# Optimization experiments

Hardware: AMD Instinct MI355X
Metric: run time of the kernel (lower is better)

## Reference

```python
import jax, jax.numpy as jnp
import numpy as np

V, E, H, B, T = 32000, 256, 512, 64, 24

def setup_inputs() -> dict:
    key = jax.random.key(0)
    ks = jax.random.split(key, 24)
    def n(k, shape, s=0.02):
        return jax.random.normal(k, shape, dtype=jnp.float32) * s
    inp = {
        "question_feat": n(ks[0], (B, H), 1.0),
        "image_feat": n(ks[1], (B, H), 1.0),
        "answer_seq": jax.random.randint(ks[2], (B, T), 0, V),
        "embedding": n(ks[3], (V, E)),
        "attn_W": n(ks[4], (H, 3 * H)),
        "attn_b": jnp.zeros((H,), jnp.float32),
        "v_W": n(ks[5], (1, H)),
        "fc_W": n(ks[6], (V, H)),
        "fc_b": jnp.zeros((V,), jnp.float32),
    }
    in_sizes = [E + 2 * H, H, H]  # layer0 sees cat(embed, context)=1280
    for l in range(3):
        inp[f"W_ih{l}"] = n(ks[7 + 4 * l], (4 * H, in_sizes[l]))
        inp[f"W_hh{l}"] = n(ks[8 + 4 * l], (4 * H, H))
        inp[f"b_ih{l}"] = jnp.zeros((4 * H,), jnp.float32)
        inp[f"b_hh{l}"] = jnp.zeros((4 * H,), jnp.float32)
    return inp

def _lstm_cell(x, h, c, W_ih, W_hh, b_ih, b_hh):
    # torch gate order: i, f, g, o
    g = x @ W_ih.T + b_ih + h @ W_hh.T + b_hh
    i, f, gg, o = jnp.split(g, 4, axis=-1)
    c_new = jax.nn.sigmoid(f) * c + jax.nn.sigmoid(i) * jnp.tanh(gg)
    h_new = jax.nn.sigmoid(o) * jnp.tanh(c_new)
    return h_new, c_new

def reference(question_feat, image_feat, answer_seq, embedding, attn_W, attn_b, v_W,
              fc_W, fc_b,
              W_ih0, W_hh0, b_ih0, b_hh0,
              W_ih1, W_hh1, b_ih1, b_hh1,
              W_ih2, W_hh2, b_ih2, b_hh2):
    combined = jnp.concatenate([question_feat, image_feat], axis=1)  # [B, 2H]
    x = embedding[answer_seq]            # [B, T, E]
    xs = jnp.swapaxes(x, 0, 1)           # [T, B, E]
    Ws = ((W_ih0, W_hh0, b_ih0, b_hh0),
          (W_ih1, W_hh1, b_ih1, b_hh1),
          (W_ih2, W_hh2, b_ih2, b_hh2))

    def step(carry, x_t):
        h, c, prev_attn = carry          # h, c: [3, B, H]; prev_attn: [B, H]
        energy = jnp.tanh(jnp.concatenate([prev_attn, combined], axis=1) @ attn_W.T + attn_b)
        aw = jax.nn.softmax(energy @ v_W.T, axis=1)  # [B, 1] (softmax over singleton, faithful to source)
        ctx = aw * combined                          # [B, 2H]
        cur = jnp.concatenate([x_t, ctx], axis=1)    # [B, E+2H]
        hs, cs = [], []
        for l in range(3):
            nh, nc = _lstm_cell(cur, h[l], c[l], *Ws[l])
            hs.append(nh); cs.append(nc); cur = nh
        logits = cur @ fc_W.T + fc_b                 # [B, V]
        return (jnp.stack(hs), jnp.stack(cs), cur), logits

    hdim = question_feat.shape[1]
    bsz = question_feat.shape[0]
    h0 = jnp.zeros((3, bsz, hdim), question_feat.dtype)
    c0 = jnp.zeros((3, bsz, hdim), question_feat.dtype)
    _, outs = jax.lax.scan(step, (h0, c0, question_feat), xs)
    return jnp.swapaxes(outs, 0, 1)  # [B, T, V]
```

## Files before the change

### kernel.cpp

```cpp
#include <hip/hip_runtime.h>
#include <hip/hip_bf16.h>
#include <stdint.h>


typedef short bf16x8 __attribute__((ext_vector_type(8)));
typedef float f32x4 __attribute__((ext_vector_type(4)));

#define NLSTM 96
#define NTILE_N 250
#define HSLOT 32768

__device__ __forceinline__ unsigned short f2b(float f) {
    uint32_t u = __builtin_bit_cast(uint32_t, f);
    uint32_t r = u + 0x7FFFu + ((u >> 16) & 1u);
    return (unsigned short)(r >> 16);
}
__device__ __forceinline__ float fsig(float x) {
    float e = __expf(-x);
    return __builtin_amdgcn_rcpf(1.0f + e);
}
__device__ __forceinline__ float ftanh(float x) {
    float e = __expf(-2.0f * x);
    return (1.0f - e) * __builtin_amdgcn_rcpf(1.0f + e);
}

__global__ __launch_bounds__(256) void prep(
    const float* __restrict__ Whh0,
    const float* __restrict__ Wih1, const float* __restrict__ Whh1,
    const float* __restrict__ Wih2, const float* __restrict__ Whh2,
    unsigned short* __restrict__ Wpk,
    const float* __restrict__ qf,
    const float* __restrict__ imf,
    const int* __restrict__ seq,
    const float* __restrict__ emb,
    unsigned short* __restrict__ X,
    unsigned int* __restrict__ flags,
    unsigned short* __restrict__ hst)
{
    int gid = blockIdx.x;
    int tid = threadIdx.x;
    if (gid < 6144) {
        int layer = gid / (32 * 64);
        int rem = gid % (32 * 64);
        int lbid = rem >> 6, r = rem & 63;
        int q = r >> 4, jj = r & 15;
        int grow = q * 512 + lbid * 16 + jj;
        int K = (layer == 0) ? 512 : 1024;
        size_t wbase = (layer == 0) ? 0
                     : (layer == 1) ? (size_t)32 * 64 * 512
                                    : (size_t)32 * 64 * 512 + (size_t)32 * 64 * 1024;
        unsigned short* dst = Wpk + wbase + ((size_t)lbid * 64 + r) * K;
        const float *s0, *s1 = nullptr;
        if (layer == 0)      { s0 = Whh0 + (size_t)grow * 512; }
        else if (layer == 1) { s0 = Wih1 + (size_t)grow * 512; s1 = Whh1 + (size_t)grow * 512; }
        else                 { s0 = Wih2 + (size_t)grow * 512; s1 = Whh2 + (size_t)grow * 512; }
        int half = tid >> 7, k4 = tid & 127;
        const float* src = (half == 0) ? s0 : s1;
        if (src) {
            f32x4 v = *(const f32x4*)&src[k4 * 4];
            unsigned short o[4];
            #pragma unroll
            for (int j = 0; j < 4; ++j) o[j] = f2b(v[j]);
            *(uint64_t*)&dst[half * 512 + k4 * 4] = *(uint64_t*)o;
        }
    } else if (gid < 7680) {
        int r = gid - 6144;
        int t = r >> 6, b = r & 63;
        int tok = seq[b * 24 + t];
        for (int e = tid; e < 1280; e += 256) {
            float v;
            if (e < 256)      v = emb[(size_t)tok * 256 + e];
            else if (e < 768) v = qf[b * 512 + (e - 256)];
            else              v = imf[b * 512 + (e - 768)];
            X[(size_t)r * 1280 + e] = f2b(v);
        }
    } else {
        int z = (gid - 7680) * 256 + tid;
        for (int i = z; i < 2304; i += 2048) flags[i] = 0u;
        unsigned int* h32 = (unsigned int*)hst;
        for (int l = 0; l < 3; ++l) {
            unsigned int* base = h32 + (size_t)l * 25 * (HSLOT / 2);
            for (int i = z; i < HSLOT / 2; i += 2048) base[i] = 0u;
        }
    }
}

__global__ __launch_bounds__(256) void gemm128(
    const unsigned short* __restrict__ A, int lda,
    const float* __restrict__ Wf, int ldb,
    int K,
    const float* __restrict__ bias0,
    const float* __restrict__ bias1,
    float* __restrict__ outf, int ldo, int mblocks, int xcdq)
{
    __shared__ unsigned short lA[128 * 72];
    __shared__ unsigned short lB[128 * 72];
    int lin = blockIdx.x;
    int wg = (lin & 7) * xcdq + (lin >> 3);
    const int m0 = (wg % mblocks) * 128, n0 = (wg / mblocks) * 128;
    const int tid = threadIdx.x;
    const int lane = tid & 63, wid = tid >> 6;
    const int wm = wid >> 1, wn = wid & 1;

    f32x4 acc[4][4] = {};

    for (int kt = 0; kt < K; kt += 64) {
        #pragma unroll
        for (int c = 0; c < 4; ++c) {
            int chunk = tid + c * 256;
            int row = chunk >> 3, kc = (chunk & 7) * 8;
            *(bf16x8*)&lA[row * 72 + kc] =
                *(const bf16x8*)&A[(size_t)(m0 + row) * lda + kt + kc];
            const float* bp = &Wf[(size_t)(n0 + row) * ldb + kt + kc];
            f32x4 v0 = *(const f32x4*)bp;
            f32x4 v1 = *(const f32x4*)(bp + 4);
            unsigned short o[8];
            #pragma unroll
            for (int x = 0; x < 4; ++x) { o[x] = f2b(v0[x]); o[4 + x] = f2b(v1[x]); }
            *(bf16x8*)&lB[row * 72 + kc] = *(bf16x8*)o;
        }
        __syncthreads();
        #pragma unroll
        for (int ks = 0; ks < 64; ks += 32) {
            int kl = ks + ((lane >> 4) << 3);
            bf16x8 af[4], bfr[4];
            #pragma unroll
            for (int i = 0; i < 4; ++i)
                af[i] = *(const bf16x8*)&lA[(wm * 64 + i * 16 + (lane & 15)) * 72 + kl];
            #pragma unroll
            for (int j = 0; j < 4; ++j)
                bfr[j] = *(const bf16x8*)&lB[(wn * 64 + j * 16 + (lane & 15)) * 72 + kl];
            #pragma unroll
            for (int i = 0; i < 4; ++i)
                #pragma unroll
                for (int j = 0; j < 4; ++j)
                    acc[i][j] = __builtin_amdgcn_mfma_f32_16x16x32_bf16(
                        af[i], bfr[j], acc[i][j], 0, 0, 0);
        }
        __syncthreads();
    }

    #pragma unroll
    for (int i = 0; i < 4; ++i) {
        #pragma unroll
        for (int j = 0; j < 4; ++j) {
            int n = n0 + wn * 64 + j * 16 + (lane & 15);
            float bias = bias0[n] + bias1[n];
            #pragma unroll
            for (int r = 0; r < 4; ++r) {
                int m = m0 + wm * 64 + i * 16 + ((lane >> 4) << 2) + r;
                outf[(size_t)m * ldo + n] = acc[i][j][r] + bias;
            }
        }
    }
}

#define ISSUE_CHUNK(buf, kb0)                                                 \
    {                                                                         \
        _Pragma("unroll")                                                     \
        for (int u_ = 0; u_ < 8; ++u_) {                                      \
            int kg_ = (kb0) + u_ * 32 + lk;                                   \
            const unsigned short* hb_ = (kg_ < 512) ? A0 : A1;                \
            int kk_ = kg_ & 511;                                              \
            const unsigned short* ap_ =                                       \
                hb_ + ((kk_ >> 4) << 10) + brow16 + (kk_ & 15);               \
            asm volatile("global_load_dwordx4 %0, %1, off"                    \
                         : "=v"(buf[u_]) : "v"(ap_) : "memory");              \
        }                                                                     \
    }
#define MFMA_CHUNK(buf, kb0)                                                  \
    {                                                                         \
        _Pragma("unroll")                                                     \
        for (int u_ = 0; u_ < 8; ++u_) {                                      \
            int ksl_ = (kb0) + u_ * 32 + lk;                                  \
            _Pragma("unroll")                                                 \
            for (int q_ = 0; q_ < 4; ++q_) {                                  \
                int gx_ = ((ksl_ >> 3) ^ (lrow & 7)) << 3;                    \
                bf16x8 bq_ = *(const bf16x8*)&lb[(q_ * 16 + lrow) * K + gx_]; \
                acc[q_] = __builtin_amdgcn_mfma_f32_16x16x32_bf16(            \
                    buf[u_], bq_, acc[q_], 0, 0, 0);                          \
            }                                                                 \
        }                                                                     \
    }
#define VM_WAIT(n) { asm volatile("s_waitcnt vmcnt(" #n ")" ::: "memory");    \
                     __builtin_amdgcn_sched_barrier(0); }
#define POLL32(fbase)                                                         \
    {                                                                         \
        const unsigned int* fp_ = (fbase);                                    \
        int idx_ = lane & 31;                                                 \
        while (true) {                                                        \
            unsigned v_ = __hip_atomic_load((unsigned int*)&fp_[idx_],        \
                                            __ATOMIC_RELAXED,                 \
                                            __HIP_MEMORY_SCOPE_AGENT);       \
            if (__all(v_ != 0u)) break;                                       \
            __builtin_amdgcn_s_sleep(1);                                      \
        }                                                                     \
    }
#define LDS_SPIN(ptr)                                                         \
    {                                                                         \
        while (__hip_atomic_load((ptr), __ATOMIC_RELAXED,                     \
                                 __HIP_MEMORY_SCOPE_WORKGROUP) == 0u)         \
            __builtin_amdgcn_s_sleep(1);                                      \
    }

__global__ __launch_bounds__(256, 1) void lstm_wave(
    const unsigned short* __restrict__ Wpk,
    const float* __restrict__ G0,
    const float* __restrict__ bih1, const float* __restrict__ bhh1,
    const float* __restrict__ bih2, const float* __restrict__ bhh2,
    unsigned short* __restrict__ hst,
    unsigned int* __restrict__ flags)
{
    extern __shared__ char smem[];
    __shared__ unsigned int syncA[24];
    __shared__ unsigned int syncB[24];
    __shared__ unsigned int lcnt[24];
    unsigned short* lb = (unsigned short*)smem;
    const int bid = blockIdx.x;
    const int tid = threadIdx.x;
    const int lane = tid & 63, w = tid >> 6;
    const int lrow = lane & 15, lk = (lane >> 4) * 8;
    const int layer = bid >> 5;
    const int lbid = bid & 31;
    const int j0 = lbid * 16;

    const int K = (layer == 0) ? 512 : 1024;
    const size_t wbase = (layer == 0) ? 0
                       : (layer == 1) ? (size_t)32 * 64 * 512
                                      : (size_t)32 * 64 * 512 + (size_t)32 * 64 * 1024;
    const unsigned short* Wblk = Wpk + wbase + (size_t)lbid * 64 * K;

    if (tid < 24) { syncA[tid] = 0u; syncB[tid] = 0u; lcnt[tid] = 0u; }
    {
        const int kshift = (layer == 0) ? 6 : 7;
        const int gm = (K >> 3) - 1;
        const int total = 64 << kshift;
        for (int idx = tid; idx < total; idx += 256) {
            int row = idx >> kshift, g = idx & gm;
            int gx = g ^ (row & 7);
            *(bf16x8*)&lb[row * K + gx * 8] =
                *(const bf16x8*)&Wblk[(size_t)row * K + g * 8];
        }
    }
    __syncthreads();

    unsigned short* hl = hst + (size_t)layer * 25 * HSLOT;
    const unsigned short* hlow =
        (layer > 0) ? hst + (size_t)(layer - 1) * 25 * HSLOT : nullptr;

    float pb[4] = {0.f, 0.f, 0.f, 0.f};
    if (layer == 1) {
        #pragma unroll
        for (int q = 0; q < 4; ++q)
            pb[q] = bih1[q * 512 + j0 + lrow] + bhh1[q * 512 + j0 + lrow];
    } else if (layer == 2) {
        #pragma unroll
        for (int q = 0; q < 4; ++q)
            pb[q] = bih2[q * 512 + j0 + lrow] + bhh2[q * 512 + j0 + lrow];
    }

    float creg[4] = {0.f, 0.f, 0.f, 0.f};
    const int brow16 = (w * 16 + lrow) << 4;

    for (int t = 0; t < 24; ++t) {
        float g0p[16];
        if (layer == 0) {
            const float* gp = G0 + (size_t)t * 64 * 2048;
            #pragma unroll
            for (int r = 0; r < 4; ++r) {
                int b = w * 16 + ((lane >> 4) << 2) + r;
                #pragma unroll
                for (int q = 0; q < 4; ++q)
                    g0p[r * 4 + q] = gp[(size_t)b * 2048 + q * 512 + j0 + lrow];
            }
        }

        const unsigned short* A0 = (layer == 0)
            ? hl + (size_t)t * HSLOT
            : hlow + (size_t)(t + 1) * HSLOT;
        const unsigned short* A1 = (layer == 0)
            ? A0
            : hl + (size_t)t * HSLOT;

        f32x4 acc[4] = {};
        bf16x8 bufA[8], bufB[8], bufC[8], bufD[8];

        if (layer == 0) {
            if (t > 0) {
                if (w == 0) {
                    POLL32(flags + (t - 1) * 32);
                    if (lane == 0)
                        __hip_atomic_store(&syncA[t], 1u, __ATOMIC_RELAXED,
                                           __HIP_MEMORY_SCOPE_WORKGROUP);
                } else {
                    LDS_SPIN(&syncA[t]);
                }
            }
            ISSUE_CHUNK(bufA, 0); ISSUE_CHUNK(bufB, 256);
            VM_WAIT(8); MFMA_CHUNK(bufA, 0);
            VM_WAIT(0); MFMA_CHUNK(bufB, 256);
        } else {
            if (t > 0) {
                if (w == 0) {
                    POLL32(flags + (layer * 24 + t - 1) * 32);
                    if (lane == 0)
                        __hip_atomic_store(&syncA[t], 1u, __ATOMIC_RELAXED,
                                           __HIP_MEMORY_SCOPE_WORKGROUP);
                } else {
                    LDS_SPIN(&syncA[t]);
                }
            }
            ISSUE_CHUNK(bufC, 512); ISSUE_CHUNK(bufD, 768);
            if (w == 0) {
                POLL32(flags + ((layer - 1) * 24 + t) * 32);
                if (lane == 0)
                    __hip_atomic_store(&syncB[t], 1u, __ATOMIC_RELAXED,
                                       __HIP_MEMORY_SCOPE_WORKGROUP);
            } else {
                LDS_SPIN(&syncB[t]);
            }
            ISSUE_CHUNK(bufA, 0); ISSUE_CHUNK(bufB, 256);
            VM_WAIT(24); MFMA_CHUNK(bufC, 512);
            VM_WAIT(16); MFMA_CHUNK(bufD, 768);
            VM_WAIT(8);  MFMA_CHUNK(bufA, 0);
            VM_WAIT(0);  MFMA_CHUNK(bufB, 256);
        }

        unsigned short* hslot = hl + (size_t)(t + 1) * HSLOT + (lbid << 10);
        #pragma unroll
        for (int r = 0; r < 4; ++r) {
            int b = w * 16 + ((lane >> 4) << 2) + r;
            float g[4];
            #pragma unroll
            for (int q = 0; q < 4; ++q) {
                float p = (layer == 0) ? g0p[r * 4 + q] : pb[q];
                g[q] = acc[q][r] + p;
            }
            float ig = fsig(g[0]);
            float fg = fsig(g[1]);
            float gg = ftanh(g[2]);
            float og = fsig(g[3]);
            float cn = fg * creg[r] + ig * gg;
            creg[r] = cn;
            float h = og * ftanh(cn);
            unsigned int hb = (unsigned int)f2b(h);
            unsigned short* hp = hslot + (b << 4) + lrow;
            asm volatile("global_store_short %0, %1, off sc1"
                         :: "v"(hp), "v"(hb) : "memory");
        }
        asm volatile("s_waitcnt vmcnt(0)" ::: "memory");
        if (lane == 0) {
            unsigned old = __hip_atomic_fetch_add(&lcnt[t], 1u, __ATOMIC_RELAXED,
                                                  __HIP_MEMORY_SCOPE_WORKGROUP);
            if (old == 3u)
                __hip_atomic_store(&flags[(layer * 24 + t) * 32 + lbid], 1u,
                                   __ATOMIC_RELAXED, __HIP_MEMORY_SCOPE_AGENT);
        }
    }
}

#define FC_ISSUE_G(buf, mtv, ks0)                                             \
    {                                                                         \
        _Pragma("unroll")                                                     \
        for (int u_ = 0; u_ < 4; ++u_) {                                      \
            _Pragma("unroll")                                                 \
            for (int i_ = 0; i_ < 4; ++i_) {                                  \
                int rl_ = i_ * 16 + lrow;                                     \
                int k_ = (ks0) + u_ * 32 + lk;                                \
                const unsigned short* ap_ = h2                                \
                    + (size_t)(2 * (mtv) + wm + 1) * HSLOT                    \
                    + ((k_ >> 4) << 10) + (rl_ << 4) + (k_ & 15);             \
                asm volatile("global_load_dwordx4 %0, %1, off"                \
                             : "=v"(buf[u_ * 4 + i_]) : "v"(ap_) : "memory"); \
            }                                                                 \
        }                                                                     \
    }
#define FC_MFMA_G(buf, ks0)                                                   \
    {                                                                         \
        _Pragma("unroll")                                                     \
        for (int u_ = 0; u_ < 4; ++u_) {                                      \
            int ks_ = (ks0) + u_ * 32 + lk;                                   \
            _Pragma("unroll")                                                 \
            for (int jj_ = 0; jj_ < 4; ++jj_) {                               \
                int row_ = wn * 64 + jj_ * 16 + lrow;                         \
                int gx_ = ((ks_ >> 3) ^ (row_ & 7)) << 3;                     \
                bf16x8 bq_ = *(const bf16x8*)&lB[row_ * 512 + gx_];           \
                _Pragma("unroll")                                             \
                for (int i_ = 0; i_ < 4; ++i_)                                \
                    acc[i_][jj_] = __builtin_amdgcn_mfma_f32_16x16x32_bf16(   \
                        buf[u_ * 4 + i_], bq_, acc[i_][jj_], 0, 0, 0);        \
            }                                                                 \
        }                                                                     \
    }
#define FC_STORES                                                             \
    {                                                                         \
        _Pragma("unroll")                                                     \
        for (int i_ = 0; i_ < 4; ++i_) {                                      \
            _Pragma("unroll")                                                 \
            for (int jj_ = 0; jj_ < 4; ++jj_) {                               \
                int n_ = n0 + wn * 64 + jj_ * 16 + lrow;                      \
                float bias_ = fcb[n_];                                        \
                _Pragma("unroll")                                             \
                for (int r_ = 0; r_ < 4; ++r_) {                              \
                    int m_ = m0 + wm * 64 + i_ * 16 + ((lane >> 4) << 2) + r_;\
                    int b_ = m_ & 63, t_ = m_ >> 6;                           \
                    __builtin_nontemporal_store(                              \
                        acc[i_][jj_][r_] + bias_,                             \
                        &out[(size_t)(b_ * 24 + t_) * 32000 + n_]);           \
                }                                                             \
            }                                                                 \
        }                                                                     \
    }

__global__ __launch_bounds__(256, 1) void fc_gemm(
    const unsigned short* __restrict__ hst,
    const float* __restrict__ fcW,
    const float* __restrict__ fcb,
    float* __restrict__ out)
{
    extern __shared__ char smem[];
    unsigned short* lB = (unsigned short*)smem;
    const int tid = threadIdx.x;
    const int lane = tid & 63, w = tid >> 6;
    const int lrow = lane & 15, lk = (lane >> 4) * 8;
    const int wm = w >> 1, wn = w & 1;
    const unsigned short* h2 = hst + (size_t)2 * 25 * HSLOT;
    const int n0 = blockIdx.x * 128;

    for (int idx = tid; idx < 128 * 64; idx += 256) {
        int row = idx >> 6, g = idx & 63;
        const float* bp = &fcW[(size_t)(n0 + row) * 512 + g * 8];
        f32x4 v0 = *(const f32x4*)bp;
        f32x4 v1 = *(const f32x4*)(bp + 4);
        unsigned short o[8];
        #pragma unroll
        for (int x = 0; x < 4; ++x) { o[x] = f2b(v0[x]); o[4 + x] = f2b(v1[x]); }
        *(bf16x8*)&lB[row * 512 + ((g ^ (row & 7)) << 3)] = *(bf16x8*)o;
    }
    __syncthreads();

    bf16x8 gA[16], gB[16];

    {
        const int m0 = 0;
        f32x4 acc[4][4] = {};
        FC_ISSUE_G(gA, 0, 0); FC_ISSUE_G(gB, 0, 128);
        VM_WAIT(16); FC_MFMA_G(gA, 0);
        FC_ISSUE_G(gA, 0, 256);
        VM_WAIT(16); FC_MFMA_G(gB, 128);
        FC_ISSUE_G(gB, 0, 384);
        VM_WAIT(16); FC_MFMA_G(gA, 256);
        VM_WAIT(0);  FC_MFMA_G(gB, 384);
        FC_ISSUE_G(gA, 1, 0); FC_ISSUE_G(gB, 1, 128);
        FC_STORES;
    }

    for (int mt = 1; mt < 12; ++mt) {
        const int m0 = mt * 128;
        f32x4 acc[4][4] = {};
        VM_WAIT(63);
        FC_MFMA_G(gA, 0);
        FC_ISSUE_G(gA, mt, 256);
        FC_MFMA_G(gB, 128);
        FC_ISSUE_G(gB, mt, 384);
        VM_WAIT(16);
        FC_MFMA_G(gA, 256);
        VM_WAIT(0);
        FC_MFMA_G(gB, 384);
        if (mt < 11) { FC_ISSUE_G(gA, mt + 1, 0); FC_ISSUE_G(gB, mt + 1, 128); }
        FC_STORES;
    }
}

extern "C" void kernel_launch(void* const* d_in, const int* in_sizes, int n_in,
                              void* d_out, int out_size, void* d_ws, size_t ws_size,
                              hipStream_t stream) {
    const float* qf  = (const float*)d_in[0];
    const float* imf = (const float*)d_in[1];
    const int*   seq = (const int*)d_in[2];
    const float* emb = (const float*)d_in[3];
    const float* fcW = (const float*)d_in[7];
    const float* fcb = (const float*)d_in[8];
    const float* Wih[3] = {(const float*)d_in[9],  (const float*)d_in[13], (const float*)d_in[17]};
    const float* Whh[3] = {(const float*)d_in[10], (const float*)d_in[14], (const float*)d_in[18]};
    const float* bih[3] = {(const float*)d_in[11], (const float*)d_in[15], (const float*)d_in[19]};
    const float* bhh[3] = {(const float*)d_in[12], (const float*)d_in[16], (const float*)d_in[20]};

    char* ws = (char*)d_ws;
    unsigned short* X     = (unsigned short*)(ws + 0);
    float*          G0    = (float*)(ws + 3932160);
    unsigned short* hst   = (unsigned short*)(ws + 16515072);
    unsigned int*   flags = (unsigned int*)(ws + 21430272);
    unsigned short* Wpk   = (unsigned short*)(ws + 21467136);

    prep<<<7688, 256, 0, stream>>>(
        Whh[0], Wih[1], Whh[1], Wih[2], Whh[2], Wpk,
        qf, imf, seq, emb, X, flags, hst);

    gemm128<<<192, 256, 0, stream>>>(
        X, 1280, Wih[0], 1280, 1280, bih[0], bhh[0], G0, 2048, 12, 192 / 8);

    lstm_wave<<<NLSTM, 256, 131072, stream>>>(
        Wpk, G0, bih[1], bhh[1], bih[2], bhh[2], hst, flags);

    fc_gemm<<<NTILE_N, 256, 131072, stream>>>(
        hst, fcW, fcb, (float*)d_out);
}
```

Measured before the change: 295.7 us.

## Fuse input gather and weight packing into consumers; stage FC outputs through LDS

The embedding/feature gather and bf16 conversion move into the layer-0 input GEMM, and the LSTM kernel converts its fp32 weights straight into LDS. This removes the large prep pass and its intermediate X and packed-weight buffers. The FC GEMM now writes its output tile through an extra 32 KB LDS staging area so each row is stored as contiguous f32x4 nontemporal writes instead of scattered scalar stores. The cost is repeated fp32 weight reads and conversions inside the GEMM and LSTM, a larger LDS footprint in fc_gemm, and extra barriers per output tile.

```diff
diff --git a/kernel.cpp b/kernel.cpp
--- a/kernel.cpp
+++ b/kernel.cpp
@@ -23,101 +23,61 @@
     float e = __expf(-2.0f * x);
     return (1.0f - e) * __builtin_amdgcn_rcpf(1.0f + e);
 }
+__device__ __forceinline__ bf16x8 cvt8(const float* p) {
+    f32x4 v0 = *(const f32x4*)p;
+    f32x4 v1 = *(const f32x4*)(p + 4);
+    unsigned short o[8];
+    #pragma unroll
+    for (int x = 0; x < 4; ++x) { o[x] = f2b(v0[x]); o[4 + x] = f2b(v1[x]); }
+    return *(bf16x8*)o;
+}
 
 __global__ __launch_bounds__(256) void prep(
-    const float* __restrict__ Whh0,
-    const float* __restrict__ Wih1, const float* __restrict__ Whh1,
-    const float* __restrict__ Wih2, const float* __restrict__ Whh2,
-    unsigned short* __restrict__ Wpk,
-    const float* __restrict__ qf,
-    const float* __restrict__ imf,
-    const int* __restrict__ seq,
-    const float* __restrict__ emb,
-    unsigned short* __restrict__ X,
     unsigned int* __restrict__ flags,
     unsigned short* __restrict__ hst)
 {
-    int gid = blockIdx.x;
-    int tid = threadIdx.x;
-    if (gid < 6144) {
-        int layer = gid / (32 * 64);
-        int rem = gid % (32 * 64);
-        int lbid = rem >> 6, r = rem & 63;
-        int q = r >> 4, jj = r & 15;
-        int grow = q * 512 + lbid * 16 + jj;
-        int K = (layer == 0) ? 512 : 1024;
-        size_t wbase = (layer == 0) ? 0
-                     : (layer == 1) ? (size_t)32 * 64 * 512
-                                    : (size_t)32 * 64 * 512 + (size_t)32 * 64 * 1024;
-        unsigned short* dst = Wpk + wbase + ((size_t)lbid * 64 + r) * K;
-        const float *s0, *s1 = nullptr;
-        if (layer == 0)      { s0 = Whh0 + (size_t)grow * 512; }
-        else if (layer == 1) { s0 = Wih1 + (size_t)grow * 512; s1 = Whh1 + (size_t)grow * 512; }
-        else                 { s0 = Wih2 + (size_t)grow * 512; s1 = Whh2 + (size_t)grow * 512; }
-        int half = tid >> 7, k4 = tid & 127;
-        const float* src = (half == 0) ? s0 : s1;
-        if (src) {
-            f32x4 v = *(const f32x4*)&src[k4 * 4];
-            unsigned short o[4];
-            #pragma unroll
-            for (int j = 0; j < 4; ++j) o[j] = f2b(v[j]);
-            *(uint64_t*)&dst[half * 512 + k4 * 4] = *(uint64_t*)o;
-        }
-    } else if (gid < 7680) {
-        int r = gid - 6144;
-        int t = r >> 6, b = r & 63;
-        int tok = seq[b * 24 + t];
-        for (int e = tid; e < 1280; e += 256) {
-            float v;
-            if (e < 256)      v = emb[(size_t)tok * 256 + e];
-            else if (e < 768) v = qf[b * 512 + (e - 256)];
-            else              v = imf[b * 512 + (e - 768)];
-            X[(size_t)r * 1280 + e] = f2b(v);
-        }
-    } else {
-        int z = (gid - 7680) * 256 + tid;
-        for (int i = z; i < 2304; i += 2048) flags[i] = 0u;
-        unsigned int* h32 = (unsigned int*)hst;
-        for (int l = 0; l < 3; ++l) {
-            unsigned int* base = h32 + (size_t)l * 25 * (HSLOT / 2);
-            for (int i = z; i < HSLOT / 2; i += 2048) base[i] = 0u;
-        }
-    }
-}
-
-__global__ __launch_bounds__(256) void gemm128(
-    const unsigned short* __restrict__ A, int lda,
-    const float* __restrict__ Wf, int ldb,
-    int K,
+    int z = blockIdx.x * 256 + threadIdx.x;
+    for (int i = z; i < 2304; i += 2048) flags[i] = 0u;
+    unsigned int* h32 = (unsigned int*)hst;
+    for (int l = 0; l < 3; ++l) {
+        unsigned int* base = h32 + (size_t)l * 25 * (HSLOT / 2);
+        for (int i = z; i < HSLOT / 2; i += 2048) base[i] = 0u;
+    }
+}
+
+__global__ __launch_bounds__(256) void g0_gemm(
+    const int* __restrict__ seq,
+    const float* __restrict__ emb,
+    const float* __restrict__ qf,
+    const float* __restrict__ imf,
+    const float* __restrict__ Wih0,
     const float* __restrict__ bias0,
     const float* __restrict__ bias1,
-    float* __restrict__ outf, int ldo, int mblocks, int xcdq)
+    float* __restrict__ outf)
 {
     __shared__ unsigned short lA[128 * 72];
     __shared__ unsigned short lB[128 * 72];
-    int lin = blockIdx.x;
-    int wg = (lin & 7) * xcdq + (lin >> 3);
-    const int m0 = (wg % mblocks) * 128, n0 = (wg / mblocks) * 128;
+    const int m0 = (blockIdx.x % 12) * 128, n0 = (blockIdx.x / 12) * 128;
     const int tid = threadIdx.x;
     const int lane = tid & 63, wid = tid >> 6;
     const int wm = wid >> 1, wn = wid & 1;
 
     f32x4 acc[4][4] = {};
 
-    for (int kt = 0; kt < K; kt += 64) {
+    for (int kt = 0; kt < 1280; kt += 64) {
         #pragma unroll
         for (int c = 0; c < 4; ++c) {
             int chunk = tid + c * 256;
             int row = chunk >> 3, kc = (chunk & 7) * 8;
-            *(bf16x8*)&lA[row * 72 + kc] =
-                *(const bf16x8*)&A[(size_t)(m0 + row) * lda + kt + kc];
-            const float* bp = &Wf[(size_t)(n0 + row) * ldb + kt + kc];
-            f32x4 v0 = *(const f32x4*)bp;
-            f32x4 v1 = *(const f32x4*)(bp + 4);
-            unsigned short o[8];
-            #pragma unroll
-            for (int x = 0; x < 4; ++x) { o[x] = f2b(v0[x]); o[4 + x] = f2b(v1[x]); }
-            *(bf16x8*)&lB[row * 72 + kc] = *(bf16x8*)o;
+            int k = kt + kc;
+            int m = m0 + row, t = m >> 6, b = m & 63;
+            const float* src;
+            if (k < 256)      src = emb + (size_t)seq[b * 24 + t] * 256 + k;
+            else if (k < 768) src = qf + b * 512 + (k - 256);
+            else              src = imf + b * 512 + (k - 768);
+            *(bf16x8*)&lA[row * 72 + kc] = cvt8(src);
+            *(bf16x8*)&lB[row * 72 + kc] =
+                cvt8(&Wih0[(size_t)(n0 + row) * 1280 + k]);
         }
         __syncthreads();
         #pragma unroll
@@ -149,7 +109,7 @@
             #pragma unroll
             for (int r = 0; r < 4; ++r) {
                 int m = m0 + wm * 64 + i * 16 + ((lane >> 4) << 2) + r;
-                outf[(size_t)m * ldo + n] = acc[i][j][r] + bias;
+                outf[(size_t)m * 2048 + n] = acc[i][j][r] + bias;
             }
         }
     }
@@ -204,7 +164,9 @@
     }
 
 __global__ __launch_bounds__(256, 1) void lstm_wave(
-    const unsigned short* __restrict__ Wpk,
+    const float* __restrict__ Whh0,
+    const float* __restrict__ Wih1, const float* __restrict__ Whh1,
+    const float* __restrict__ Wih2, const float* __restrict__ Whh2,
     const float* __restrict__ G0,
     const float* __restrict__ bih1, const float* __restrict__ bhh1,
     const float* __restrict__ bih2, const float* __restrict__ bhh2,
@@ -225,10 +187,8 @@
     const int j0 = lbid * 16;
 
     const int K = (layer == 0) ? 512 : 1024;
-    const size_t wbase = (layer == 0) ? 0
-                       : (layer == 1) ? (size_t)32 * 64 * 512
-                                      : (size_t)32 * 64 * 512 + (size_t)32 * 64 * 1024;
-    const unsigned short* Wblk = Wpk + wbase + (size_t)lbid * 64 * K;
+    const float* WihL = (layer == 1) ? Wih1 : Wih2;
+    const float* WhhL = (layer == 0) ? Whh0 : (layer == 1) ? Whh1 : Whh2;
 
     if (tid < 24) { syncA[tid] = 0u; syncB[tid] = 0u; lcnt[tid] = 0u; }
     {
@@ -237,9 +197,13 @@
         const int total = 64 << kshift;
         for (int idx = tid; idx < total; idx += 256) {
             int row = idx >> kshift, g = idx & gm;
-            int gx = g ^ (row & 7);
-            *(bf16x8*)&lb[row * K + gx * 8] =
-                *(const bf16x8*)&Wblk[(size_t)row * K + g * 8];
+            int q = row >> 4, jj = row & 15;
+            int grow = q * 512 + lbid * 16 + jj;
+            const float* src;
+            if (layer == 0)   src = WhhL + (size_t)grow * 512 + g * 8;
+            else if (g < 64)  src = WihL + (size_t)grow * 512 + g * 8;
+            else              src = WhhL + (size_t)grow * 512 + (g - 64) * 8;
+            *(bf16x8*)&lb[row * K + ((g ^ (row & 7)) << 3)] = cvt8(src);
         }
     }
     __syncthreads();
@@ -392,25 +356,6 @@
             }                                                                 \
         }                                                                     \
     }
-#define FC_STORES                                                             \
-    {                                                                         \
-        _Pragma("unroll")                                                     \
-        for (int i_ = 0; i_ < 4; ++i_) {                                      \
-            _Pragma("unroll")                                                 \
-            for (int jj_ = 0; jj_ < 4; ++jj_) {                               \
-                int n_ = n0 + wn * 64 + jj_ * 16 + lrow;                      \
-                float bias_ = fcb[n_];                                        \
-                _Pragma("unroll")                                             \
-                for (int r_ = 0; r_ < 4; ++r_) {                              \
-                    int m_ = m0 + wm * 64 + i_ * 16 + ((lane >> 4) << 2) + r_;\
-                    int b_ = m_ & 63, t_ = m_ >> 6;                           \
-                    __builtin_nontemporal_store(                              \
-                        acc[i_][jj_][r_] + bias_,                             \
-                        &out[(size_t)(b_ * 24 + t_) * 32000 + n_]);           \
-                }                                                             \
-            }                                                                 \
-        }                                                                     \
-    }
 
 __global__ __launch_bounds__(256, 1) void fc_gemm(
     const unsigned short* __restrict__ hst,
@@ -420,6 +365,7 @@
 {
     extern __shared__ char smem[];
     unsigned short* lB = (unsigned short*)smem;
+    float* ltr = (float*)(smem + 131072);
     const int tid = threadIdx.x;
     const int lane = tid & 63, w = tid >> 6;
     const int lrow = lane & 15, lk = (lane >> 4) * 8;
@@ -429,46 +375,51 @@
 
     for (int idx = tid; idx < 128 * 64; idx += 256) {
         int row = idx >> 6, g = idx & 63;
-        const float* bp = &fcW[(size_t)(n0 + row) * 512 + g * 8];
-        f32x4 v0 = *(const f32x4*)bp;
-        f32x4 v1 = *(const f32x4*)(bp + 4);
-        unsigned short o[8];
-        #pragma unroll
-        for (int x = 0; x < 4; ++x) { o[x] = f2b(v0[x]); o[4 + x] = f2b(v1[x]); }
-        *(bf16x8*)&lB[row * 512 + ((g ^ (row & 7)) << 3)] = *(bf16x8*)o;
-    }
+        *(bf16x8*)&lB[row * 512 + ((g ^ (row & 7)) << 3)] =
+            cvt8(&fcW[(size_t)(n0 + row) * 512 + g * 8]);
+    }
+    const int cl = (tid & 31) * 4;
+    f32x4 breg = *(const f32x4*)&fcb[n0 + cl];
     __syncthreads();
 
     bf16x8 gA[16], gB[16];
-
-    {
-        const int m0 = 0;
+    FC_ISSUE_G(gA, 0, 0); FC_ISSUE_G(gB, 0, 128);
+
+    for (int mt = 0; mt < 12; ++mt) {
+        const int m0 = mt * 128;
         f32x4 acc[4][4] = {};
-        FC_ISSUE_G(gA, 0, 0); FC_ISSUE_G(gB, 0, 128);
         VM_WAIT(16); FC_MFMA_G(gA, 0);
-        FC_ISSUE_G(gA, 0, 256);
+        FC_ISSUE_G(gA, mt, 256);
         VM_WAIT(16); FC_MFMA_G(gB, 128);
-        FC_ISSUE_G(gB, 0, 384);
+        FC_ISSUE_G(gB, mt, 384);
         VM_WAIT(16); FC_MFMA_G(gA, 256);
         VM_WAIT(0);  FC_MFMA_G(gB, 384);
-        FC_ISSUE_G(gA, 1, 0); FC_ISSUE_G(gB, 1, 128);
-        FC_STORES;
-    }
-
-    for (int mt = 1; mt < 12; ++mt) {
-        const int m0 = mt * 128;
-        f32x4 acc[4][4] = {};
-        VM_WAIT(63);
-        FC_MFMA_G(gA, 0);
-        FC_ISSUE_G(gA, mt, 256);
-        FC_MFMA_G(gB, 128);
-        FC_ISSUE_G(gB, mt, 384);
-        VM_WAIT(16);
-        FC_MFMA_G(gA, 256);
-        VM_WAIT(0);
-        FC_MFMA_G(gB, 384);
         if (mt < 11) { FC_ISSUE_G(gA, mt + 1, 0); FC_ISSUE_G(gB, mt + 1, 128); }
-        FC_STORES;
+
+        #pragma unroll
+        for (int half = 0; half < 2; ++half) {
+            if (wm == half) {
+                #pragma unroll
+                for (int i = 0; i < 4; ++i)
+                    #pragma unroll
+                    for (int jj = 0; jj < 4; ++jj)
+                        #pragma unroll
+                        for (int r = 0; r < 4; ++r)
+                            ltr[(i * 16 + ((lane >> 4) << 2) + r) * 128
+                                + wn * 64 + jj * 16 + lrow] = acc[i][jj][r];
+            }
+            __syncthreads();
+            const int t_ = 2 * mt + half;
+            #pragma unroll
+            for (int rr = 0; rr < 8; ++rr) {
+                int row = rr * 8 + (tid >> 5);
+                f32x4 v = *(const f32x4*)&ltr[row * 128 + cl];
+                v += breg;
+                __builtin_nontemporal_store(v,
+                    (f32x4*)&out[(size_t)(row * 24 + t_) * 32000 + n0 + cl]);
+            }
+            __syncthreads();
+        }
     }
 }
 
@@ -487,22 +438,19 @@
     const float* bhh[3] = {(const float*)d_in[12], (const float*)d_in[16], (const float*)d_in[20]};
 
     char* ws = (char*)d_ws;
-    unsigned short* X     = (unsigned short*)(ws + 0);
-    float*          G0    = (float*)(ws + 3932160);
-    unsigned short* hst   = (unsigned short*)(ws + 16515072);
-    unsigned int*   flags = (unsigned int*)(ws + 21430272);
-    unsigned short* Wpk   = (unsigned short*)(ws + 21467136);
-
-    prep<<<7688, 256, 0, stream>>>(
-        Whh[0], Wih[1], Whh[1], Wih[2], Whh[2], Wpk,
-        qf, imf, seq, emb, X, flags, hst);
-
-    gemm128<<<192, 256, 0, stream>>>(
-        X, 1280, Wih[0], 1280, 1280, bih[0], bhh[0], G0, 2048, 12, 192 / 8);
+    float*          G0    = (float*)(ws + 0);
+    unsigned short* hst   = (unsigned short*)(ws + 12582912);
+    unsigned int*   flags = (unsigned int*)(ws + 17498112);
+
+    prep<<<8, 256, 0, stream>>>(flags, hst);
+
+    g0_gemm<<<192, 256, 0, stream>>>(
+        seq, emb, qf, imf, Wih[0], bih[0], bhh[0], G0);
 
     lstm_wave<<<NLSTM, 256, 131072, stream>>>(
-        Wpk, G0, bih[1], bhh[1], bih[2], bhh[2], hst, flags);
-
-    fc_gemm<<<NTILE_N, 256, 131072, stream>>>(
+        Whh[0], Wih[1], Whh[1], Wih[2], Whh[2],
+        G0, bih[1], bhh[1], bih[2], bhh[2], hst, flags);
+
+    fc_gemm<<<NTILE_N, 256, 163840, stream>>>(
         hst, fcW, fcb, (float*)d_out);
 }
```

Result: slower. 311.8 us (+5.4%).
